# Performance work log

Measured on AMD Instinct MI355X. Metric: run time of the kernel, lower is better.

Reference implementation:

```python
import jax, jax.numpy as jnp
import numpy as np

NUM_OPS, B, T, D = 8, 8, 512, 1024


def setup_inputs() -> dict:
    key = jax.random.key(0)
    k1, k2, k3, k4 = jax.random.split(key, 4)
    x = jax.random.normal(k1, (B, T, D), dtype=jnp.float32)
    W = jax.random.normal(k2, (NUM_OPS, D, D), dtype=jnp.float32) * 0.02
    b = jnp.zeros((NUM_OPS, D), dtype=jnp.float32)
    logits = 0.001 * jax.random.normal(k3, (NUM_OPS,), dtype=jnp.float32)
    # uniform noise for Gumbel sampling (matches tf.random.uniform in sample_without_replacement)
    u = jax.random.uniform(k4, (NUM_OPS,), dtype=jnp.float32, minval=1e-6, maxval=1.0 - 1e-6)
    return {"x": x, "W": W, "b": b, "logits": logits, "u": u}


def reference(x, W, b, logits, u):
    # weights = softmax(logits); gumbel top-1 over log(weights) == log_softmax(logits)
    gumbel = -jnp.log(-jnp.log(u))
    idx = jnp.argmax(jax.nn.log_softmax(logits) + gumbel)
    # forward of ops_times_mask_binary: sum over ON ops (num_on_samples=1 -> single op)
    out = jnp.einsum('btd,de->bte', x, W[idx]) + b[idx]  # [B,T,D]
    return out
```

## Files before the change

### kernel.cpp

```cpp
#include <hip/hip_runtime.h>

typedef unsigned short u16;
typedef unsigned int u32;
typedef __attribute__((ext_vector_type(8))) short bf16x8;
typedef __attribute__((ext_vector_type(4))) float f32x4;

#define NUM_OPS 8
#define M_DIM 4096
#define K_DIM 1024
#define N_DIM 1024
#define BK 64
#define KITERS (K_DIM / BK)


__device__ __forceinline__ u16 f2b(float f) {
  union { float f; u32 u; } v; v.f = f;
  u32 r = v.u + 0x7fffu + ((v.u >> 16) & 1u);
  return (u16)(r >> 16);
}

__device__ __forceinline__ u32 pk2(float a, float b) {
  return (u32)f2b(a) | ((u32)f2b(b) << 16);
}

__device__ __forceinline__ int compute_idx(const float* __restrict__ logits,
                                           const float* __restrict__ u) {
  int best = 0; float bv = -3.4e38f;
#pragma unroll
  for (int i = 0; i < NUM_OPS; ++i) {
    float v = logits[i] - logf(-logf(u[i]));
    if (v > bv) { bv = v; best = i; }
  }
  return best;
}

__device__ __forceinline__ void gld_lds16(const void* g, void* l) {
  __builtin_amdgcn_global_load_lds(
      (__attribute__((address_space(1))) void*)(g),
      (__attribute__((address_space(3))) void*)(unsigned)(unsigned long long)(l),
      16, 0, 0);
}

__global__ void prep_kernel(const float* __restrict__ x, const float* __restrict__ W,
                            const float* __restrict__ logits, const float* __restrict__ u,
                            u16* __restrict__ xb, u16* __restrict__ wt) {
  const int tid = threadIdx.x;
  const int bid = blockIdx.x;
  if (bid < 2048) {
    const int chunk = bid * 4 + (tid >> 6), l = tid & 63;
    const int mtile = chunk >> 5, ktile = chunk & 31;
    const float* src = x + (size_t)(mtile * 16 + (l & 15)) * K_DIM
                         + ktile * 32 + (l >> 4) * 8;
    float4 f0 = *(const float4*)(src);
    float4 f1 = *(const float4*)(src + 4);
    uint4 p;
    p.x = pk2(f0.x, f0.y); p.y = pk2(f0.z, f0.w);
    p.z = pk2(f1.x, f1.y); p.w = pk2(f1.z, f1.w);
    *(uint4*)(xb + (size_t)chunk * 512 + l * 8) = p;
  } else {
    __shared__ u16 t[64][66];
    const int wb = bid - 2048;
    const int kt = wb >> 4, nt = wb & 15;
    const int idx = compute_idx(logits, u);
    const float* Wi = W + (size_t)idx * K_DIM * N_DIM;
#pragma unroll
    for (int it = 0; it < 16; ++it) {
      int i = it * 256 + tid;
      int r = i >> 6, c = i & 63;
      t[r][c] = f2b(Wi[(size_t)(kt * 64 + r) * N_DIM + nt * 64 + c]);
    }
    __syncthreads();
#pragma unroll
    for (int it = 0; it < 2; ++it) {
      int s = it * 256 + tid;
      int c = s >> 6, l = s & 63;
      int ntl = c & 3, ktl = c >> 2;
      int kb = ktl * 32 + (l >> 4) * 8, nn = ntl * 16 + (l & 15);
      uint4 p;
      p.x = (u32)t[kb + 0][nn] | ((u32)t[kb + 1][nn] << 16);
      p.y = (u32)t[kb + 2][nn] | ((u32)t[kb + 3][nn] << 16);
      p.z = (u32)t[kb + 4][nn] | ((u32)t[kb + 5][nn] << 16);
      p.w = (u32)t[kb + 6][nn] | ((u32)t[kb + 7][nn] << 16);
      int chunk = (nt * 4 + ntl) * 32 + (kt * 2 + ktl);
      *(uint4*)(wt + (size_t)chunk * 512 + l * 8) = p;
    }
  }
}

__global__ __launch_bounds__(256) void gemm_kernel(
    const u16* __restrict__ xb, const u16* __restrict__ wt,
    const float* __restrict__ bvec, const float* __restrict__ logits,
    const float* __restrict__ u, float* __restrict__ out) {
  __shared__ u16 sm[2][24 * 512];

  const int tid = threadIdx.x;
  const int w = tid >> 6, L = tid & 63;
  const int bid = blockIdx.x;
  const int mb = (bid & 7) * 8 + (bid >> 6);
  const int nb = (bid >> 3) & 7;

  const u16* gsrc[6];
  int lofs[6];
#pragma unroll
  for (int j = 0; j < 6; ++j) {
    int item = 6 * w + j;
    if (item < 8) {
      int mt = item >> 1, dk = item & 1;
      gsrc[j] = xb + ((size_t)((mb * 4 + mt) * 32 + dk)) * 512 + L * 8;
    } else {
      int t = item - 8, nt = t >> 1, dk = t & 1;
      gsrc[j] = wt + ((size_t)((nb * 8 + nt) * 32 + dk)) * 512 + L * 8;
    }
    lofs[j] = item * 512 + L * 8;
  }

  const int wm = w & 1, wn = w >> 1;
  int aoff[2][2], boff[4][2];
#pragma unroll
  for (int f = 0; f < 2; ++f)
#pragma unroll
    for (int dk = 0; dk < 2; ++dk)
      aoff[f][dk] = ((2 * wm + f) * 2 + dk) * 512 + L * 8;
#pragma unroll
  for (int t = 0; t < 4; ++t)
#pragma unroll
    for (int dk = 0; dk < 2; ++dk)
      boff[t][dk] = (8 + (4 * wn + t) * 2 + dk) * 512 + L * 8;

  f32x4 acc[2][4] = {};

#pragma unroll
  for (int j = 0; j < 6; ++j) gld_lds16(gsrc[j], &sm[0][lofs[j]]);

  for (int kk = 0; kk < KITERS; ++kk) {
    const int cur = kk & 1, nxt = cur ^ 1;
    __syncthreads();

    if (kk + 1 < KITERS) {
      const int ko = (kk + 1) * 1024;
#pragma unroll
      for (int j = 0; j < 6; ++j) gld_lds16(gsrc[j] + ko, &sm[nxt][lofs[j]]);
    }

    bf16x8 af[2][2], bf[4][2];
#pragma unroll
    for (int f = 0; f < 2; ++f)
#pragma unroll
      for (int dk = 0; dk < 2; ++dk)
        af[f][dk] = *(const bf16x8*)(&sm[cur][aoff[f][dk]]);
#pragma unroll
    for (int t = 0; t < 4; ++t)
#pragma unroll
      for (int dk = 0; dk < 2; ++dk)
        bf[t][dk] = *(const bf16x8*)(&sm[cur][boff[t][dk]]);
#pragma unroll
    for (int dk = 0; dk < 2; ++dk)
#pragma unroll
      for (int f = 0; f < 2; ++f)
#pragma unroll
        for (int t = 0; t < 4; ++t)
          acc[f][t] = __builtin_amdgcn_mfma_f32_16x16x32_bf16(
              af[f][dk], bf[t][dk], acc[f][t], 0, 0, 0);
  }

  const int idx = compute_idx(logits, u);
  const float* bi = bvec + (size_t)idx * N_DIM;
#pragma unroll
  for (int f = 0; f < 2; ++f) {
    int row = mb * 64 + 32 * wm + 16 * f + (L >> 4) * 4;
#pragma unroll
    for (int t = 0; t < 4; ++t) {
      int col = nb * 128 + 64 * wn + 16 * t + (L & 15);
      float bv = bi[col];
#pragma unroll
      for (int r = 0; r < 4; ++r)
        out[(size_t)(row + r) * N_DIM + col] = acc[f][t][r] + bv;
    }
  }
}


extern "C" void kernel_launch(void* const* d_in, const int* in_sizes, int n_in,
                              void* d_out, int out_size, void* d_ws, size_t ws_size,
                              hipStream_t stream) {
  const float* x      = (const float*)d_in[0];
  const float* W      = (const float*)d_in[1];
  const float* bvec   = (const float*)d_in[2];
  const float* logits = (const float*)d_in[3];
  const float* u      = (const float*)d_in[4];
  float* out = (float*)d_out;

  u16* xb = (u16*)d_ws;
  u16* wt = (u16*)d_ws + (size_t)M_DIM * K_DIM;

  prep_kernel<<<2048 + 256, 256, 0, stream>>>(x, W, logits, u, xb, wt);
  gemm_kernel<<<512, 256, 0, stream>>>(xb, wt, bvec, logits, u, out);
}
```

Baseline: 105.9 us.

## Fuse fp32-to-bf16 conversion of x into GEMM with register-staged pipelining

```diff
diff --git a/kernel.cpp b/kernel.cpp
--- a/kernel.cpp
+++ b/kernel.cpp
@@ -11,6 +11,8 @@
 #define N_DIM 1024
 #define BK 64
 #define KITERS (K_DIM / BK)
+#define UNROLL _Pragma("unroll")
+
 
 
 __device__ __forceinline__ u16 f2b(float f) {
@@ -19,14 +21,16 @@
   return (u16)(r >> 16);
 }
 
-__device__ __forceinline__ u32 pk2(float a, float b) {
-  return (u32)f2b(a) | ((u32)f2b(b) << 16);
+__device__ __forceinline__ u32 cvtpk(float lo, float hi) {
+  u32 r;
+  asm("v_cvt_pk_bf16_f32 %0, %1, %2" : "=v"(r) : "v"(lo), "v"(hi));
+  return r;
 }
 
 __device__ __forceinline__ int compute_idx(const float* __restrict__ logits,
                                            const float* __restrict__ u) {
   int best = 0; float bv = -3.4e38f;
-#pragma unroll
+UNROLL
   for (int i = 0; i < NUM_OPS; ++i) {
     float v = logits[i] - logf(-logf(u[i]));
     if (v > bv) { bv = v; best = i; }
@@ -41,54 +45,41 @@
       16, 0, 0);
 }
 
-__global__ void prep_kernel(const float* __restrict__ x, const float* __restrict__ W,
-                            const float* __restrict__ logits, const float* __restrict__ u,
-                            u16* __restrict__ xb, u16* __restrict__ wt) {
+__global__ void prep_kernel(const float* __restrict__ W,
+                            const float* __restrict__ logits,
+                            const float* __restrict__ u,
+                            u16* __restrict__ wt) {
+  __shared__ u16 t[64][66];
   const int tid = threadIdx.x;
-  const int bid = blockIdx.x;
-  if (bid < 2048) {
-    const int chunk = bid * 4 + (tid >> 6), l = tid & 63;
-    const int mtile = chunk >> 5, ktile = chunk & 31;
-    const float* src = x + (size_t)(mtile * 16 + (l & 15)) * K_DIM
-                         + ktile * 32 + (l >> 4) * 8;
-    float4 f0 = *(const float4*)(src);
-    float4 f1 = *(const float4*)(src + 4);
+  const int wb = blockIdx.x;
+  const int kt = wb >> 4, nt = wb & 15;
+  const int idx = compute_idx(logits, u);
+  const float* Wi = W + (size_t)idx * K_DIM * N_DIM;
+UNROLL
+  for (int it = 0; it < 16; ++it) {
+    int i = it * 256 + tid;
+    int r = i >> 6, c = i & 63;
+    t[r][c] = f2b(Wi[(size_t)(kt * 64 + r) * N_DIM + nt * 64 + c]);
+  }
+  __syncthreads();
+UNROLL
+  for (int it = 0; it < 2; ++it) {
+    int s = it * 256 + tid;
+    int c = s >> 6, l = s & 63;
+    int ntl = c & 3, ktl = c >> 2;
+    int kb = ktl * 32 + (l >> 4) * 8, nn = ntl * 16 + (l & 15);
     uint4 p;
-    p.x = pk2(f0.x, f0.y); p.y = pk2(f0.z, f0.w);
-    p.z = pk2(f1.x, f1.y); p.w = pk2(f1.z, f1.w);
-    *(uint4*)(xb + (size_t)chunk * 512 + l * 8) = p;
-  } else {
-    __shared__ u16 t[64][66];
-    const int wb = bid - 2048;
-    const int kt = wb >> 4, nt = wb & 15;
-    const int idx = compute_idx(logits, u);
-    const float* Wi = W + (size_t)idx * K_DIM * N_DIM;
-#pragma unroll
-    for (int it = 0; it < 16; ++it) {
-      int i = it * 256 + tid;
-      int r = i >> 6, c = i & 63;
-      t[r][c] = f2b(Wi[(size_t)(kt * 64 + r) * N_DIM + nt * 64 + c]);
-    }
-    __syncthreads();
-#pragma unroll
-    for (int it = 0; it < 2; ++it) {
-      int s = it * 256 + tid;
-      int c = s >> 6, l = s & 63;
-      int ntl = c & 3, ktl = c >> 2;
-      int kb = ktl * 32 + (l >> 4) * 8, nn = ntl * 16 + (l & 15);
-      uint4 p;
-      p.x = (u32)t[kb + 0][nn] | ((u32)t[kb + 1][nn] << 16);
-      p.y = (u32)t[kb + 2][nn] | ((u32)t[kb + 3][nn] << 16);
-      p.z = (u32)t[kb + 4][nn] | ((u32)t[kb + 5][nn] << 16);
-      p.w = (u32)t[kb + 6][nn] | ((u32)t[kb + 7][nn] << 16);
-      int chunk = (nt * 4 + ntl) * 32 + (kt * 2 + ktl);
-      *(uint4*)(wt + (size_t)chunk * 512 + l * 8) = p;
-    }
+    p.x = (u32)t[kb + 0][nn] | ((u32)t[kb + 1][nn] << 16);
+    p.y = (u32)t[kb + 2][nn] | ((u32)t[kb + 3][nn] << 16);
+    p.z = (u32)t[kb + 4][nn] | ((u32)t[kb + 5][nn] << 16);
+    p.w = (u32)t[kb + 6][nn] | ((u32)t[kb + 7][nn] << 16);
+    int chunk = (nt * 4 + ntl) * 32 + (kt * 2 + ktl);
+    *(uint4*)(wt + (size_t)chunk * 512 + l * 8) = p;
   }
 }
 
 __global__ __launch_bounds__(256) void gemm_kernel(
-    const u16* __restrict__ xb, const u16* __restrict__ wt,
+    const float* __restrict__ x, const u16* __restrict__ wt,
     const float* __restrict__ bvec, const float* __restrict__ logits,
     const float* __restrict__ u, float* __restrict__ out) {
   __shared__ u16 sm[2][24 * 512];
@@ -99,80 +90,117 @@
   const int mb = (bid & 7) * 8 + (bid >> 6);
   const int nb = (bid >> 3) & 7;
 
-  const u16* gsrc[6];
-  int lofs[6];
-#pragma unroll
-  for (int j = 0; j < 6; ++j) {
-    int item = 6 * w + j;
-    if (item < 8) {
-      int mt = item >> 1, dk = item & 1;
-      gsrc[j] = xb + ((size_t)((mb * 4 + mt) * 32 + dk)) * 512 + L * 8;
-    } else {
-      int t = item - 8, nt = t >> 1, dk = t & 1;
-      gsrc[j] = wt + ((size_t)((nb * 8 + nt) * 32 + dk)) * 512 + L * 8;
-    }
-    lofs[j] = item * 512 + L * 8;
+  const float* asrc[2];
+  int alofs[2];
+UNROLL
+  for (int j = 0; j < 2; ++j) {
+    int s = tid + j * 256;
+    int chunk = s >> 6, l = s & 63;
+    asrc[j] = x + (size_t)(mb * 64 + (chunk >> 1) * 16 + (l & 15)) * K_DIM
+                + (chunk & 1) * 32 + (l >> 4) * 8;
+    alofs[j] = chunk * 512 + l * 8;
+  }
+
+  const u16* bsrc[4];
+  int blofs[4];
+UNROLL
+  for (int j = 0; j < 4; ++j) {
+    int item = 4 * w + j;
+    int nt = item >> 1, dk = item & 1;
+    bsrc[j] = wt + ((size_t)((nb * 8 + nt) * 32 + dk)) * 512 + L * 8;
+    blofs[j] = (8 + item) * 512 + L * 8;
   }
 
   const int wm = w & 1, wn = w >> 1;
   int aoff[2][2], boff[4][2];
-#pragma unroll
+UNROLL
   for (int f = 0; f < 2; ++f)
-#pragma unroll
+UNROLL
     for (int dk = 0; dk < 2; ++dk)
       aoff[f][dk] = ((2 * wm + f) * 2 + dk) * 512 + L * 8;
-#pragma unroll
+UNROLL
   for (int t = 0; t < 4; ++t)
-#pragma unroll
+UNROLL
     for (int dk = 0; dk < 2; ++dk)
       boff[t][dk] = (8 + (4 * wn + t) * 2 + dk) * 512 + L * 8;
 
   f32x4 acc[2][4] = {};
-
-#pragma unroll
-  for (int j = 0; j < 6; ++j) gld_lds16(gsrc[j], &sm[0][lofs[j]]);
-
-  for (int kk = 0; kk < KITERS; ++kk) {
-    const int cur = kk & 1, nxt = cur ^ 1;
+  float4 gA[2][2], gB[2][2];
+
+#define LOAD_A(dst, kk) do {                                          \
+  UNROLL                                                              \
+  for (int j_ = 0; j_ < 2; ++j_) {                                    \
+    dst[j_][0] = *(const float4*)(asrc[j_] + (kk) * BK);              \
+    dst[j_][1] = *(const float4*)(asrc[j_] + (kk) * BK + 4);          \
+  } } while (0)
+
+#define WRITE_A(src, bufi) do {                                       \
+  UNROLL                                                              \
+  for (int j_ = 0; j_ < 2; ++j_) {                                    \
+    uint4 p_;                                                         \
+    p_.x = cvtpk(src[j_][0].x, src[j_][0].y);                         \
+    p_.y = cvtpk(src[j_][0].z, src[j_][0].w);                         \
+    p_.z = cvtpk(src[j_][1].x, src[j_][1].y);                         \
+    p_.w = cvtpk(src[j_][1].z, src[j_][1].w);                         \
+    *(uint4*)(&sm[bufi][alofs[j_]]) = p_;                             \
+  } } while (0)
+
+#define STAGE_B(kk, bufi) do {                                        \
+  const int ko_ = (kk) * 1024;                                        \
+  UNROLL                                                              \
+  for (int j_ = 0; j_ < 4; ++j_)                                      \
+    gld_lds16(bsrc[j_] + ko_, &sm[bufi][blofs[j_]]);                  \
+  } while (0)
+
+#define COMPUTE(cur) do {                                             \
+  bf16x8 af_[2][2], bf_[4][2];                                        \
+  UNROLL                                                              \
+  for (int f_ = 0; f_ < 2; ++f_)                                      \
+    UNROLL                                                            \
+    for (int dk_ = 0; dk_ < 2; ++dk_)                                 \
+      af_[f_][dk_] = *(const bf16x8*)(&sm[cur][aoff[f_][dk_]]);       \
+  UNROLL                                                              \
+  for (int t_ = 0; t_ < 4; ++t_)                                      \
+    UNROLL                                                            \
+    for (int dk_ = 0; dk_ < 2; ++dk_)                                 \
+      bf_[t_][dk_] = *(const bf16x8*)(&sm[cur][boff[t_][dk_]]);       \
+  UNROLL                                                              \
+  for (int dk_ = 0; dk_ < 2; ++dk_)                                   \
+    UNROLL                                                            \
+    for (int f_ = 0; f_ < 2; ++f_)                                    \
+      UNROLL                                                          \
+      for (int t_ = 0; t_ < 4; ++t_)                                  \
+        acc[f_][t_] = __builtin_amdgcn_mfma_f32_16x16x32_bf16(        \
+            af_[f_][dk_], bf_[t_][dk_], acc[f_][t_], 0, 0, 0);        \
+  } while (0)
+
+  LOAD_A(gA, 0);
+  STAGE_B(0, 0);
+  WRITE_A(gA, 0);
+  LOAD_A(gB, 1);
+
+  for (int kk = 0; kk < KITERS; kk += 2) {
     __syncthreads();
-
-    if (kk + 1 < KITERS) {
-      const int ko = (kk + 1) * 1024;
-#pragma unroll
-      for (int j = 0; j < 6; ++j) gld_lds16(gsrc[j] + ko, &sm[nxt][lofs[j]]);
-    }
-
-    bf16x8 af[2][2], bf[4][2];
-#pragma unroll
-    for (int f = 0; f < 2; ++f)
-#pragma unroll
-      for (int dk = 0; dk < 2; ++dk)
-        af[f][dk] = *(const bf16x8*)(&sm[cur][aoff[f][dk]]);
-#pragma unroll
-    for (int t = 0; t < 4; ++t)
-#pragma unroll
-      for (int dk = 0; dk < 2; ++dk)
-        bf[t][dk] = *(const bf16x8*)(&sm[cur][boff[t][dk]]);
-#pragma unroll
-    for (int dk = 0; dk < 2; ++dk)
-#pragma unroll
-      for (int f = 0; f < 2; ++f)
-#pragma unroll
-        for (int t = 0; t < 4; ++t)
-          acc[f][t] = __builtin_amdgcn_mfma_f32_16x16x32_bf16(
-              af[f][dk], bf[t][dk], acc[f][t], 0, 0, 0);
+    if (kk + 1 < KITERS) { STAGE_B(kk + 1, 1); WRITE_A(gB, 1); }
+    if (kk + 2 < KITERS) LOAD_A(gA, kk + 2);
+    COMPUTE(0);
+
+    __syncthreads();
+    if (kk + 2 < KITERS) { STAGE_B(kk + 2, 0); WRITE_A(gA, 0); }
+    if (kk + 3 < KITERS) LOAD_A(gB, kk + 3);
+    COMPUTE(1);
   }
 
   const int idx = compute_idx(logits, u);
   const float* bi = bvec + (size_t)idx * N_DIM;
-#pragma unroll
+UNROLL
   for (int f = 0; f < 2; ++f) {
     int row = mb * 64 + 32 * wm + 16 * f + (L >> 4) * 4;
-#pragma unroll
+UNROLL
     for (int t = 0; t < 4; ++t) {
       int col = nb * 128 + 64 * wn + 16 * t + (L & 15);
       float bv = bi[col];
-#pragma unroll
+UNROLL
       for (int r = 0; r < 4; ++r)
         out[(size_t)(row + r) * N_DIM + col] = acc[f][t][r] + bv;
     }
@@ -190,9 +218,8 @@
   const float* u      = (const float*)d_in[4];
   float* out = (float*)d_out;
 
-  u16* xb = (u16*)d_ws;
-  u16* wt = (u16*)d_ws + (size_t)M_DIM * K_DIM;
-
-  prep_kernel<<<2048 + 256, 256, 0, stream>>>(x, W, logits, u, xb, wt);
-  gemm_kernel<<<512, 256, 0, stream>>>(xb, wt, bvec, logits, u, out);
-}
+  u16* wt = (u16*)d_ws;
+
+  prep_kernel<<<256, 256, 0, stream>>>(W, logits, u, wt);
+  gemm_kernel<<<512, 256, 0, stream>>>(x, wt, bvec, logits, u, out);
+}
```

Result: slower. 117.6 us (+11.1%).

## Load GEMM fragments directly from global into registers, drop LDS staging

Applied to the files above, without the earlier changes.

```diff
diff --git a/kernel.cpp b/kernel.cpp
--- a/kernel.cpp
+++ b/kernel.cpp
@@ -9,8 +9,9 @@
 #define M_DIM 4096
 #define K_DIM 1024
 #define N_DIM 1024
-#define BK 64
-#define KITERS (K_DIM / BK)
+#define KITERS 16
+#define UNROLL _Pragma("unroll")
+
 
 
 __device__ __forceinline__ u16 f2b(float f) {
@@ -26,19 +27,12 @@
 __device__ __forceinline__ int compute_idx(const float* __restrict__ logits,
                                            const float* __restrict__ u) {
   int best = 0; float bv = -3.4e38f;
-#pragma unroll
+UNROLL
   for (int i = 0; i < NUM_OPS; ++i) {
     float v = logits[i] - logf(-logf(u[i]));
     if (v > bv) { bv = v; best = i; }
   }
   return best;
-}
-
-__device__ __forceinline__ void gld_lds16(const void* g, void* l) {
-  __builtin_amdgcn_global_load_lds(
-      (__attribute__((address_space(1))) void*)(g),
-      (__attribute__((address_space(3))) void*)(unsigned)(unsigned long long)(l),
-      16, 0, 0);
 }
 
 __global__ void prep_kernel(const float* __restrict__ x, const float* __restrict__ W,
@@ -63,14 +57,14 @@
     const int kt = wb >> 4, nt = wb & 15;
     const int idx = compute_idx(logits, u);
     const float* Wi = W + (size_t)idx * K_DIM * N_DIM;
-#pragma unroll
+UNROLL
     for (int it = 0; it < 16; ++it) {
       int i = it * 256 + tid;
       int r = i >> 6, c = i & 63;
       t[r][c] = f2b(Wi[(size_t)(kt * 64 + r) * N_DIM + nt * 64 + c]);
     }
     __syncthreads();
-#pragma unroll
+UNROLL
     for (int it = 0; it < 2; ++it) {
       int s = it * 256 + tid;
       int c = s >> 6, l = s & 63;
@@ -91,88 +85,64 @@
     const u16* __restrict__ xb, const u16* __restrict__ wt,
     const float* __restrict__ bvec, const float* __restrict__ logits,
     const float* __restrict__ u, float* __restrict__ out) {
-  __shared__ u16 sm[2][24 * 512];
-
   const int tid = threadIdx.x;
   const int w = tid >> 6, L = tid & 63;
   const int bid = blockIdx.x;
   const int mb = (bid & 7) * 8 + (bid >> 6);
   const int nb = (bid >> 3) & 7;
+  const int wm = w & 1, wn = w >> 1;
 
-  const u16* gsrc[6];
-  int lofs[6];
-#pragma unroll
-  for (int j = 0; j < 6; ++j) {
-    int item = 6 * w + j;
-    if (item < 8) {
-      int mt = item >> 1, dk = item & 1;
-      gsrc[j] = xb + ((size_t)((mb * 4 + mt) * 32 + dk)) * 512 + L * 8;
-    } else {
-      int t = item - 8, nt = t >> 1, dk = t & 1;
-      gsrc[j] = wt + ((size_t)((nb * 8 + nt) * 32 + dk)) * 512 + L * 8;
-    }
-    lofs[j] = item * 512 + L * 8;
-  }
-
-  const int wm = w & 1, wn = w >> 1;
-  int aoff[2][2], boff[4][2];
-#pragma unroll
-  for (int f = 0; f < 2; ++f)
-#pragma unroll
-    for (int dk = 0; dk < 2; ++dk)
-      aoff[f][dk] = ((2 * wm + f) * 2 + dk) * 512 + L * 8;
-#pragma unroll
-  for (int t = 0; t < 4; ++t)
-#pragma unroll
-    for (int dk = 0; dk < 2; ++dk)
-      boff[t][dk] = (8 + (4 * wn + t) * 2 + dk) * 512 + L * 8;
+  const u16* abase = xb + (size_t)((mb * 4 + 2 * wm) * 32) * 512 + L * 8;
+  const u16* bbase = wt + (size_t)((nb * 8 + wn * 4) * 32) * 512 + L * 8;
 
   f32x4 acc[2][4] = {};
+  bf16x8 a0[2][2], b0[4][2], a1[2][2], b1[4][2];
 
-#pragma unroll
-  for (int j = 0; j < 6; ++j) gld_lds16(gsrc[j], &sm[0][lofs[j]]);
+#define LOADF(A, B, kk) do {                                              \
+  UNROLL                                                                  \
+  for (int f_ = 0; f_ < 2; ++f_)                                          \
+    UNROLL                                                                \
+    for (int d_ = 0; d_ < 2; ++d_)                                        \
+      A[f_][d_] = *(const bf16x8*)(abase + (f_ * 32 + (kk) * 2 + d_) * 512); \
+  UNROLL                                                                  \
+  for (int t_ = 0; t_ < 4; ++t_)                                          \
+    UNROLL                                                                \
+    for (int d_ = 0; d_ < 2; ++d_)                                        \
+      B[t_][d_] = *(const bf16x8*)(bbase + (t_ * 32 + (kk) * 2 + d_) * 512); \
+} while (0)
 
-  for (int kk = 0; kk < KITERS; ++kk) {
-    const int cur = kk & 1, nxt = cur ^ 1;
-    __syncthreads();
+#define MFMAS(A, B) do {                                                  \
+  UNROLL                                                                  \
+  for (int d_ = 0; d_ < 2; ++d_)                                          \
+    UNROLL                                                                \
+    for (int f_ = 0; f_ < 2; ++f_)                                        \
+      UNROLL                                                              \
+      for (int t_ = 0; t_ < 4; ++t_)                                      \
+        acc[f_][t_] = __builtin_amdgcn_mfma_f32_16x16x32_bf16(            \
+            A[f_][d_], B[t_][d_], acc[f_][t_], 0, 0, 0);                  \
+} while (0)
 
-    if (kk + 1 < KITERS) {
-      const int ko = (kk + 1) * 1024;
-#pragma unroll
-      for (int j = 0; j < 6; ++j) gld_lds16(gsrc[j] + ko, &sm[nxt][lofs[j]]);
-    }
+  LOADF(a0, b0, 0);
+  LOADF(a1, b1, 1);
 
-    bf16x8 af[2][2], bf[4][2];
-#pragma unroll
-    for (int f = 0; f < 2; ++f)
-#pragma unroll
-      for (int dk = 0; dk < 2; ++dk)
-        af[f][dk] = *(const bf16x8*)(&sm[cur][aoff[f][dk]]);
-#pragma unroll
-    for (int t = 0; t < 4; ++t)
-#pragma unroll
-      for (int dk = 0; dk < 2; ++dk)
-        bf[t][dk] = *(const bf16x8*)(&sm[cur][boff[t][dk]]);
-#pragma unroll
-    for (int dk = 0; dk < 2; ++dk)
-#pragma unroll
-      for (int f = 0; f < 2; ++f)
-#pragma unroll
-        for (int t = 0; t < 4; ++t)
-          acc[f][t] = __builtin_amdgcn_mfma_f32_16x16x32_bf16(
-              af[f][dk], bf[t][dk], acc[f][t], 0, 0, 0);
+UNROLL
+  for (int kk = 0; kk < KITERS; kk += 2) {
+    MFMAS(a0, b0);
+    if (kk + 2 < KITERS) LOADF(a0, b0, kk + 2);
+    MFMAS(a1, b1);
+    if (kk + 3 < KITERS) LOADF(a1, b1, kk + 3);
   }
 
   const int idx = compute_idx(logits, u);
   const float* bi = bvec + (size_t)idx * N_DIM;
-#pragma unroll
+UNROLL
   for (int f = 0; f < 2; ++f) {
     int row = mb * 64 + 32 * wm + 16 * f + (L >> 4) * 4;
-#pragma unroll
+UNROLL
     for (int t = 0; t < 4; ++t) {
       int col = nb * 128 + 64 * wn + 16 * t + (L & 15);
       float bv = bi[col];
-#pragma unroll
+UNROLL
       for (int r = 0; r < 4; ++r)
         out[(size_t)(row + r) * N_DIM + col] = acc[f][t][r] + bv;
     }
```

Result: slower. 109.9 us (+3.7%).

## Fuse prep and GEMM into one cooperative kernel with grid sync

Applied to the files above, without the earlier changes.

```diff
diff --git a/kernel.cpp b/kernel.cpp
--- a/kernel.cpp
+++ b/kernel.cpp
@@ -1,4 +1,7 @@
 #include <hip/hip_runtime.h>
+#include <hip/hip_cooperative_groups.h>
+
+namespace cg = cooperative_groups;
 
 typedef unsigned short u16;
 typedef unsigned int u32;
@@ -9,8 +12,9 @@
 #define M_DIM 4096
 #define K_DIM 1024
 #define N_DIM 1024
-#define BK 64
-#define KITERS (K_DIM / BK)
+#define KITERS 16
+#define UNROLL _Pragma("unroll")
+
 
 
 __device__ __forceinline__ u16 f2b(float f) {
@@ -26,7 +30,7 @@
 __device__ __forceinline__ int compute_idx(const float* __restrict__ logits,
                                            const float* __restrict__ u) {
   int best = 0; float bv = -3.4e38f;
-#pragma unroll
+UNROLL
   for (int i = 0; i < NUM_OPS; ++i) {
     float v = logits[i] - logf(-logf(u[i]));
     if (v > bv) { bv = v; best = i; }
@@ -39,6 +43,168 @@
       (__attribute__((address_space(1))) void*)(g),
       (__attribute__((address_space(3))) void*)(unsigned)(unsigned long long)(l),
       16, 0, 0);
+}
+
+__device__ __forceinline__ void do_xchunks(const float* __restrict__ x,
+                                           u16* __restrict__ xb,
+                                           int mb, int nb, int w, int l) {
+UNROLL
+  for (int it = 0; it < 4; ++it) {
+    const int chunk = mb * 128 + nb * 16 + it * 4 + w;
+    const int mtile = chunk >> 5, ktile = chunk & 31;
+    const float* src = x + (size_t)(mtile * 16 + (l & 15)) * K_DIM
+                         + ktile * 32 + (l >> 4) * 8;
+    float4 f0 = *(const float4*)(src);
+    float4 f1 = *(const float4*)(src + 4);
+    uint4 p;
+    p.x = pk2(f0.x, f0.y); p.y = pk2(f0.z, f0.w);
+    p.z = pk2(f1.x, f1.y); p.w = pk2(f1.z, f1.w);
+    *(uint4*)(xb + (size_t)chunk * 512 + l * 8) = p;
+  }
+}
+
+__device__ __forceinline__ void do_wtile(const float* __restrict__ W,
+                                         const float* __restrict__ logits,
+                                         const float* __restrict__ u,
+                                         u16* __restrict__ wt,
+                                         u16 (*t)[66], int wb, int tid) {
+  const int kt = wb >> 4, nt = wb & 15;
+  const int idx = compute_idx(logits, u);
+  const float* Wi = W + (size_t)idx * K_DIM * N_DIM;
+UNROLL
+  for (int it = 0; it < 16; ++it) {
+    int i = it * 256 + tid;
+    int r = i >> 6, c = i & 63;
+    t[r][c] = f2b(Wi[(size_t)(kt * 64 + r) * N_DIM + nt * 64 + c]);
+  }
+  __syncthreads();
+UNROLL
+  for (int it = 0; it < 2; ++it) {
+    int s = it * 256 + tid;
+    int c = s >> 6, l = s & 63;
+    int ntl = c & 3, ktl = c >> 2;
+    int kb = ktl * 32 + (l >> 4) * 8, nn = ntl * 16 + (l & 15);
+    uint4 p;
+    p.x = (u32)t[kb + 0][nn] | ((u32)t[kb + 1][nn] << 16);
+    p.y = (u32)t[kb + 2][nn] | ((u32)t[kb + 3][nn] << 16);
+    p.z = (u32)t[kb + 4][nn] | ((u32)t[kb + 5][nn] << 16);
+    p.w = (u32)t[kb + 6][nn] | ((u32)t[kb + 7][nn] << 16);
+    int chunk = (nt * 4 + ntl) * 32 + (kt * 2 + ktl);
+    *(uint4*)(wt + (size_t)chunk * 512 + l * 8) = p;
+  }
+}
+
+__device__ __forceinline__ void gemm_body(
+    const u16* __restrict__ xb, const u16* __restrict__ wt,
+    const float* __restrict__ bvec, const float* __restrict__ logits,
+    const float* __restrict__ u, float* __restrict__ out,
+    u16 (*sm)[24 * 512], int tid, int bid) {
+  const int w = tid >> 6, L = tid & 63;
+  const int mb = (bid & 7) * 8 + (bid >> 6);
+  const int nb = (bid >> 3) & 7;
+
+  const u16* gsrc[6];
+  int lofs[6];
+UNROLL
+  for (int j = 0; j < 6; ++j) {
+    int item = 6 * w + j;
+    if (item < 8) {
+      int mt = item >> 1, dk = item & 1;
+      gsrc[j] = xb + ((size_t)((mb * 4 + mt) * 32 + dk)) * 512 + L * 8;
+    } else {
+      int t = item - 8, nt = t >> 1, dk = t & 1;
+      gsrc[j] = wt + ((size_t)((nb * 8 + nt) * 32 + dk)) * 512 + L * 8;
+    }
+    lofs[j] = item * 512 + L * 8;
+  }
+
+  const int wm = w & 1, wn = w >> 1;
+  int aoff[2][2], boff[4][2];
+UNROLL
+  for (int f = 0; f < 2; ++f)
+UNROLL
+    for (int dk = 0; dk < 2; ++dk)
+      aoff[f][dk] = ((2 * wm + f) * 2 + dk) * 512 + L * 8;
+UNROLL
+  for (int t = 0; t < 4; ++t)
+UNROLL
+    for (int dk = 0; dk < 2; ++dk)
+      boff[t][dk] = (8 + (4 * wn + t) * 2 + dk) * 512 + L * 8;
+
+  f32x4 acc[2][4] = {};
+
+UNROLL
+  for (int j = 0; j < 6; ++j) gld_lds16(gsrc[j], &sm[0][lofs[j]]);
+
+  for (int kk = 0; kk < KITERS; ++kk) {
+    const int cur = kk & 1, nxt = cur ^ 1;
+    __syncthreads();
+
+    if (kk + 1 < KITERS) {
+      const int ko = (kk + 1) * 1024;
+UNROLL
+      for (int j = 0; j < 6; ++j) gld_lds16(gsrc[j] + ko, &sm[nxt][lofs[j]]);
+    }
+
+    bf16x8 af[2][2], bf[4][2];
+UNROLL
+    for (int f = 0; f < 2; ++f)
+UNROLL
+      for (int dk = 0; dk < 2; ++dk)
+        af[f][dk] = *(const bf16x8*)(&sm[cur][aoff[f][dk]]);
+UNROLL
+    for (int t = 0; t < 4; ++t)
+UNROLL
+      for (int dk = 0; dk < 2; ++dk)
+        bf[t][dk] = *(const bf16x8*)(&sm[cur][boff[t][dk]]);
+UNROLL
+    for (int dk = 0; dk < 2; ++dk)
+UNROLL
+      for (int f = 0; f < 2; ++f)
+UNROLL
+        for (int t = 0; t < 4; ++t)
+          acc[f][t] = __builtin_amdgcn_mfma_f32_16x16x32_bf16(
+              af[f][dk], bf[t][dk], acc[f][t], 0, 0, 0);
+  }
+
+  const int idx = compute_idx(logits, u);
+  const float* bi = bvec + (size_t)idx * N_DIM;
+UNROLL
+  for (int f = 0; f < 2; ++f) {
+    int row = mb * 64 + 32 * wm + 16 * f + (L >> 4) * 4;
+UNROLL
+    for (int t = 0; t < 4; ++t) {
+      int col = nb * 128 + 64 * wn + 16 * t + (L & 15);
+      float bv = bi[col];
+UNROLL
+      for (int r = 0; r < 4; ++r)
+        out[(size_t)(row + r) * N_DIM + col] = acc[f][t][r] + bv;
+    }
+  }
+}
+
+__global__ __launch_bounds__(256, 2) void fused_kernel(
+    const float* __restrict__ x, const float* __restrict__ W,
+    const float* __restrict__ bvec, const float* __restrict__ logits,
+    const float* __restrict__ u, u16* __restrict__ xb, u16* __restrict__ wt,
+    float* __restrict__ out) {
+  __shared__ u16 sm[2][24 * 512];
+
+  const int tid = threadIdx.x;
+  const int bid = blockIdx.x;
+  const int w = tid >> 6, L = tid & 63;
+  const int mb = (bid & 7) * 8 + (bid >> 6);
+  const int nb = (bid >> 3) & 7;
+
+  do_xchunks(x, xb, mb, nb, w, L);
+  if (bid < 256)
+    do_wtile(W, logits, u, wt, (u16(*)[66]) & sm[0][0], bid, tid);
+
+  __threadfence();
+  cg::this_grid().sync();
+  __threadfence();
+
+  gemm_body(xb, wt, bvec, logits, u, out, sm, tid, bid);
 }
 
 __global__ void prep_kernel(const float* __restrict__ x, const float* __restrict__ W,
@@ -59,31 +225,7 @@
     *(uint4*)(xb + (size_t)chunk * 512 + l * 8) = p;
   } else {
     __shared__ u16 t[64][66];
-    const int wb = bid - 2048;
-    const int kt = wb >> 4, nt = wb & 15;
-    const int idx = compute_idx(logits, u);
-    const float* Wi = W + (size_t)idx * K_DIM * N_DIM;
-#pragma unroll
-    for (int it = 0; it < 16; ++it) {
-      int i = it * 256 + tid;
-      int r = i >> 6, c = i & 63;
-      t[r][c] = f2b(Wi[(size_t)(kt * 64 + r) * N_DIM + nt * 64 + c]);
-    }
-    __syncthreads();
-#pragma unroll
-    for (int it = 0; it < 2; ++it) {
-      int s = it * 256 + tid;
-      int c = s >> 6, l = s & 63;
-      int ntl = c & 3, ktl = c >> 2;
-      int kb = ktl * 32 + (l >> 4) * 8, nn = ntl * 16 + (l & 15);
-      uint4 p;
-      p.x = (u32)t[kb + 0][nn] | ((u32)t[kb + 1][nn] << 16);
-      p.y = (u32)t[kb + 2][nn] | ((u32)t[kb + 3][nn] << 16);
-      p.z = (u32)t[kb + 4][nn] | ((u32)t[kb + 5][nn] << 16);
-      p.w = (u32)t[kb + 6][nn] | ((u32)t[kb + 7][nn] << 16);
-      int chunk = (nt * 4 + ntl) * 32 + (kt * 2 + ktl);
-      *(uint4*)(wt + (size_t)chunk * 512 + l * 8) = p;
-    }
+    do_wtile(W, logits, u, wt, t, bid - 2048, tid);
   }
 }
 
@@ -92,91 +234,7 @@
     const float* __restrict__ bvec, const float* __restrict__ logits,
     const float* __restrict__ u, float* __restrict__ out) {
   __shared__ u16 sm[2][24 * 512];
-
-  const int tid = threadIdx.x;
-  const int w = tid >> 6, L = tid & 63;
-  const int bid = blockIdx.x;
-  const int mb = (bid & 7) * 8 + (bid >> 6);
-  const int nb = (bid >> 3) & 7;
-
-  const u16* gsrc[6];
-  int lofs[6];
-#pragma unroll
-  for (int j = 0; j < 6; ++j) {
-    int item = 6 * w + j;
-    if (item < 8) {
-      int mt = item >> 1, dk = item & 1;
-      gsrc[j] = xb + ((size_t)((mb * 4 + mt) * 32 + dk)) * 512 + L * 8;
-    } else {
-      int t = item - 8, nt = t >> 1, dk = t & 1;
-      gsrc[j] = wt + ((size_t)((nb * 8 + nt) * 32 + dk)) * 512 + L * 8;
-    }
-    lofs[j] = item * 512 + L * 8;
-  }
-
-  const int wm = w & 1, wn = w >> 1;
-  int aoff[2][2], boff[4][2];
-#pragma unroll
-  for (int f = 0; f < 2; ++f)
-#pragma unroll
-    for (int dk = 0; dk < 2; ++dk)
-      aoff[f][dk] = ((2 * wm + f) * 2 + dk) * 512 + L * 8;
-#pragma unroll
-  for (int t = 0; t < 4; ++t)
-#pragma unroll
-    for (int dk = 0; dk < 2; ++dk)
-      boff[t][dk] = (8 + (4 * wn + t) * 2 + dk) * 512 + L * 8;
-
-  f32x4 acc[2][4] = {};
-
-#pragma unroll
-  for (int j = 0; j < 6; ++j) gld_lds16(gsrc[j], &sm[0][lofs[j]]);
-
-  for (int kk = 0; kk < KITERS; ++kk) {
-    const int cur = kk & 1, nxt = cur ^ 1;
-    __syncthreads();
-
-    if (kk + 1 < KITERS) {
-      const int ko = (kk + 1) * 1024;
-#pragma unroll
-      for (int j = 0; j < 6; ++j) gld_lds16(gsrc[j] + ko, &sm[nxt][lofs[j]]);
-    }
-
-    bf16x8 af[2][2], bf[4][2];
-#pragma unroll
-    for (int f = 0; f < 2; ++f)
-#pragma unroll
-      for (int dk = 0; dk < 2; ++dk)
-        af[f][dk] = *(const bf16x8*)(&sm[cur][aoff[f][dk]]);
-#pragma unroll
-    for (int t = 0; t < 4; ++t)
-#pragma unroll
-      for (int dk = 0; dk < 2; ++dk)
-        bf[t][dk] = *(const bf16x8*)(&sm[cur][boff[t][dk]]);
-#pragma unroll
-    for (int dk = 0; dk < 2; ++dk)
-#pragma unroll
-      for (int f = 0; f < 2; ++f)
-#pragma unroll
-        for (int t = 0; t < 4; ++t)
-          acc[f][t] = __builtin_amdgcn_mfma_f32_16x16x32_bf16(
-              af[f][dk], bf[t][dk], acc[f][t], 0, 0, 0);
-  }
-
-  const int idx = compute_idx(logits, u);
-  const float* bi = bvec + (size_t)idx * N_DIM;
-#pragma unroll
-  for (int f = 0; f < 2; ++f) {
-    int row = mb * 64 + 32 * wm + 16 * f + (L >> 4) * 4;
-#pragma unroll
-    for (int t = 0; t < 4; ++t) {
-      int col = nb * 128 + 64 * wn + 16 * t + (L & 15);
-      float bv = bi[col];
-#pragma unroll
-      for (int r = 0; r < 4; ++r)
-        out[(size_t)(row + r) * N_DIM + col] = acc[f][t][r] + bv;
-    }
-  }
+  gemm_body(xb, wt, bvec, logits, u, out, sm, threadIdx.x, blockIdx.x);
 }
 
 
@@ -193,6 +251,12 @@
   u16* xb = (u16*)d_ws;
   u16* wt = (u16*)d_ws + (size_t)M_DIM * K_DIM;
 
-  prep_kernel<<<2048 + 256, 256, 0, stream>>>(x, W, logits, u, xb, wt);
-  gemm_kernel<<<512, 256, 0, stream>>>(xb, wt, bvec, logits, u, out);
-}
+  void* args[] = {(void*)&x, (void*)&W, (void*)&bvec, (void*)&logits,
+                  (void*)&u, (void*)&xb, (void*)&wt, (void*)&out};
+  hipError_t e = hipLaunchCooperativeKernel((const void*)fused_kernel,
+                                            dim3(512), dim3(256), args, 0, stream);
+  if (e != hipSuccess) {
+    prep_kernel<<<2048 + 256, 256, 0, stream>>>(x, W, logits, u, xb, wt);
+    gemm_kernel<<<512, 256, 0, stream>>>(xb, wt, bvec, logits, u, out);
+  }
+}
```

Result: slower. 260.8 us (+146.3%).
